# Kernel optimization log

Measured on AMD Instinct MI355X. Metric: run time of the kernel, lower is better.

## Reference

```python
import jax, jax.numpy as jnp
import numpy as np

NEG_INF = -1e9


def setup_inputs() -> dict:
    key = jax.random.key(0)
    k1, k2, k3 = jax.random.split(key, 3)
    B, N, F_IN, F_OUT = 8, 4096, 128, 64
    h = jax.random.normal(k1, (B, N, F_IN), dtype=jnp.float32)
    # xavier_uniform with gain=1.414 on [F_IN, F_OUT]
    limit = 1.414 * np.sqrt(6.0 / (F_IN + F_OUT))
    W = jax.random.uniform(k2, (F_IN, F_OUT), dtype=jnp.float32, minval=-limit, maxval=limit)
    adj = jax.random.randint(k3, (N, N), 0, 2, dtype=jnp.int32)
    return {"h": h, "W": W, "adj": adj}


def reference(h, W, adj):
    # h: [B, N, F_in], W: [F_in, F_out], adj: [N, N]
    F_out = W.shape[1]
    Wh = jnp.einsum('bnf,fo->bno', h, W)                      # [B, N, F_out]
    scores = jnp.einsum('bnd,bmd->bnm', Wh, Wh) / np.sqrt(F_out).astype(np.float32)
    attention = jnp.where(adj[None, :, :] > 0, scores, NEG_INF)
    attention = jax.nn.softmax(attention, axis=2)             # [B, N, N]
    # dropout p=0.0 / eval mode -> identity
    h_prime = jnp.einsum('bnm,bmd->bnd', attention, Wh)       # [B, N, F_out]
    return jax.nn.elu(h_prime)  # concat=True path
```

## Files before the change

### kernel.cpp

```cpp
#include <hip/hip_runtime.h>

typedef _Float16 half8  __attribute__((ext_vector_type(8)));
typedef _Float16 half4v __attribute__((ext_vector_type(4)));
typedef float    float4v __attribute__((ext_vector_type(4)));

#define N_ 4096
#define B_ 8
#define D_ 64
#define F_ 128

__global__ __launch_bounds__(256) void pack_adj_kernel(const int4* __restrict__ adj4,
                                                       unsigned long long* __restrict__ bits) {
  __shared__ unsigned char nib[256];
  const int t = threadIdx.x;
  int4 v = adj4[(size_t)blockIdx.x * 256 + t];
  unsigned n = (v.x > 0 ? 1u : 0u) | (v.y > 0 ? 2u : 0u) |
               (v.z > 0 ? 4u : 0u) | (v.w > 0 ? 8u : 0u);
  nib[t] = (unsigned char)n;
  __syncthreads();
  if (t < 16) {
    const unsigned char* p = &nib[t * 16];
    unsigned long long wv = 0;
#pragma unroll
    for (int i = 0; i < 16; ++i) wv |= (unsigned long long)p[i] << (4 * i);
    bits[(size_t)blockIdx.x * 16 + t] = wv;
  }
}

__global__ __launch_bounds__(256) void wh_kernel(const float* __restrict__ h,
                                                 const float* __restrict__ W,
                                                 _Float16* __restrict__ Wh16,
                                                 _Float16* __restrict__ WhT16) {
  __shared__ __align__(16) float    hs[64][132];
  __shared__ __align__(16) _Float16 wt[64][132];
  __shared__ __align__(16) _Float16 otile[64][72];
  const int t = threadIdx.x;
  const int rowbase = blockIdx.x * 64;
  const float4v* hg = (const float4v*)(h + (size_t)rowbase * F_);
#pragma unroll
  for (int k = 0; k < 8; ++k) {
    int i4 = t + k * 256;
    float4v v = hg[i4];
    int r = i4 >> 5, c4 = (i4 & 31) * 4;
    *(float4v*)&hs[r][c4] = v;
  }
#pragma unroll
  for (int k = 0; k < 8; ++k) {
    int i4 = t + k * 256;
    float4v v = ((const float4v*)W)[i4];
    int f = i4 >> 4, c4 = (i4 & 15) * 4;
    wt[c4 + 0][f] = (_Float16)v[0];
    wt[c4 + 1][f] = (_Float16)v[1];
    wt[c4 + 2][f] = (_Float16)v[2];
    wt[c4 + 3][f] = (_Float16)v[3];
  }
  __syncthreads();
  const int w = t >> 6, lane = t & 63;
  const int r0 = w * 16;
  float acc[16];
#pragma unroll
  for (int i = 0; i < 16; ++i) acc[i] = 0.f;
#pragma unroll 4
  for (int f4 = 0; f4 < 32; ++f4) {
    half4v wv = *(half4v*)&wt[lane][f4 * 4];
    float w0 = (float)wv[0], w1 = (float)wv[1], w2 = (float)wv[2], w3 = (float)wv[3];
#pragma unroll
    for (int i = 0; i < 16; ++i) {
      float4v hv = *(float4v*)&hs[r0 + i][f4 * 4];
      acc[i] += hv[0] * w0 + hv[1] * w1 + hv[2] * w2 + hv[3] * w3;
    }
  }
#pragma unroll
  for (int i = 0; i < 16; ++i) {
    _Float16 hv = (_Float16)acc[i];
    Wh16[(size_t)(rowbase + r0 + i) * D_ + lane] = hv;
    otile[r0 + i][lane] = hv;
  }
  __syncthreads();
  const int dl = t >> 2, k0t = (t & 3) * 16;
  half8 o0, o1;
#pragma unroll
  for (int i = 0; i < 8; ++i) o0[i] = otile[k0t + i][dl];
#pragma unroll
  for (int i = 0; i < 8; ++i) o1[i] = otile[k0t + 8 + i][dl];
  const int b = rowbase >> 12, n0 = rowbase & 4095;
  _Float16* dst = WhT16 + ((size_t)(b * D_ + dl)) * N_ + n0 + k0t;
  *(half8*)dst       = o0;
  *(half8*)(dst + 8) = o1;
}

__global__ __launch_bounds__(512, 4) void attn_kernel(
    const unsigned long long* __restrict__ bits,
    const _Float16* __restrict__ Wh,
    const _Float16* __restrict__ WhT,
    float* __restrict__ out) {
  __shared__ __align__(16) char lds[81920];
  const int tid  = threadIdx.x;
  const int w    = tid >> 6;
  const int lane = tid & 63;
  const int g    = lane >> 4;
  const int c    = lane & 15;
  const int qi   = w & 3;
  const int s    = w >> 2;
  const int bid  = blockIdx.x;
  const int b    = bid >> 6;
  const int q0b  = (bid & 63) * 64;
  const int q0w  = q0b + qi * 16;

  const _Float16* Whb  = Wh  + (size_t)b * N_ * D_;
  const _Float16* WhTb = WhT + (size_t)b * D_ * N_;
  char* Kbase = lds + s * 16384;
  char* Vbase = lds + 32768 + s * 16384;
  char* Pb    = lds + 65536 + w * 2048;

  const int e0  = (qi * 2 + 0) * 64 + lane;
  const int e1  = (qi * 2 + 1) * 64 + lane;
  const int r0e = e0 >> 3, s0e = (e0 & 7) ^ (r0e & 7);
  const int r1e = e1 >> 3, s1e = (e1 & 7) ^ (r1e & 7);

  half8 qf[2];
#pragma unroll
  for (int ds = 0; ds < 2; ++ds) {
    half8 v = *(const half8*)(Whb + (size_t)(q0w + c) * D_ + ds * 32 + g * 8);
    qf[ds] = v * (_Float16)0.18033688f;
  }

  float4v o_acc[4];
#pragma unroll
  for (int d = 0; d < 4; ++d) o_acc[d] = (float4v){0.f, 0.f, 0.f, 0.f};
  float mrow = -1e30f, lrow = 0.f;

  const unsigned long long* bq = bits + (size_t)(q0w + c) * 64 + s * 32;

  int k0n = (s * 32) * 64;
  half8 ka = *(const half8*)(Whb + (size_t)(k0n + r0e) * D_ + s0e * 8);
  half8 kb = *(const half8*)(Whb + (size_t)(k0n + r1e) * D_ + s1e * 8);
  half8 va = *(const half8*)(WhTb + (size_t)r0e * N_ + k0n + s0e * 8);
  half8 vb = *(const half8*)(WhTb + (size_t)r1e * N_ + k0n + s1e * 8);
  unsigned long long bw = bq[0];
  *(half8*)(Kbase + e0 * 16) = ka;
  *(half8*)(Kbase + e1 * 16) = kb;
  *(half8*)(Vbase + e0 * 16) = va;
  *(half8*)(Vbase + e1 * 16) = vb;
  __syncthreads();

  for (int t = 0; t < 32; ++t) {
    const int cur = (t & 1) * 8192, nxt = 8192 - cur;
    const _Float16* Kc = (const _Float16*)(Kbase + cur);
    const _Float16* Vc = (const _Float16*)(Vbase + cur);

    const int t1 = (t + 1 < 32) ? t + 1 : 31;
    k0n = (s * 32 + t1) * 64;
    ka = *(const half8*)(Whb + (size_t)(k0n + r0e) * D_ + s0e * 8);
    kb = *(const half8*)(Whb + (size_t)(k0n + r1e) * D_ + s1e * 8);
    va = *(const half8*)(WhTb + (size_t)r0e * N_ + k0n + s0e * 8);
    vb = *(const half8*)(WhTb + (size_t)r1e * N_ + k0n + s1e * 8);
    unsigned long long bwn = bq[t1];

    float4v sac[4];
#pragma unroll
    for (int st = 0; st < 4; ++st) {
      const _Float16* kr = Kc + (st * 16 + c) * 64;
      half8 kf0 = *(const half8*)(kr + ((g       ^ (c & 7)) * 8));
      half8 kf1 = *(const half8*)(kr + (((g + 4) ^ (c & 7)) * 8));
      float4v z = (float4v){0.f, 0.f, 0.f, 0.f};
      z = __builtin_amdgcn_mfma_f32_16x16x32_f16(kf0, qf[0], z, 0, 0, 0);
      z = __builtin_amdgcn_mfma_f32_16x16x32_f16(kf1, qf[1], z, 0, 0, 0);
      sac[st] = z;
    }

    float tmax = -1e30f;
#pragma unroll
    for (int st = 0; st < 4; ++st) {
      unsigned wb = (unsigned)(bw >> (st * 16 + g * 4));
#pragma unroll
      for (int j = 0; j < 4; ++j) {
        float v = (wb & (1u << j)) ? sac[st][j] : -1e9f;
        sac[st][j] = v;
        tmax = fmaxf(tmax, v);
      }
    }
    tmax = fmaxf(tmax, __shfl_xor(tmax, 16));
    tmax = fmaxf(tmax, __shfl_xor(tmax, 32));

    float mnew  = fmaxf(mrow, tmax);
    float alpha = exp2f(mrow - mnew);
    mrow = mnew;
    lrow *= alpha;
#pragma unroll
    for (int j = 0; j < 4; ++j) {
      float aj = __shfl(alpha, (lane & 48) | (g * 4 + j));
#pragma unroll
      for (int d = 0; d < 4; ++d) o_acc[d][j] *= aj;
    }

#pragma unroll
    for (int st = 0; st < 4; ++st) {
      float p0 = exp2f(sac[st][0] - mrow);
      float p1 = exp2f(sac[st][1] - mrow);
      float p2 = exp2f(sac[st][2] - mrow);
      float p3 = exp2f(sac[st][3] - mrow);
      lrow += (p0 + p1) + (p2 + p3);
      uint2 pr;
      pr.x = __builtin_bit_cast(unsigned, __builtin_amdgcn_cvt_pkrtz(p0, p1));
      pr.y = __builtin_bit_cast(unsigned, __builtin_amdgcn_cvt_pkrtz(p2, p3));
      const int cell = st * 2 + (g >> 1);
      *(uint2*)(Pb + (cell * 16 + c) * 16 + (g & 1) * 8) = pr;
    }

#pragma unroll
    for (int ks = 0; ks < 2; ++ks) {
      half8 af = *(const half8*)(Pb + ((ks * 4 + g) * 16 + c) * 16);
#pragma unroll
      for (int d = 0; d < 4; ++d) {
        const int vrow = d * 16 + c;
        half8 vf = *(const half8*)(Vc + vrow * 64 + (((ks * 4 + g) ^ (c & 7)) * 8));
        o_acc[d] = __builtin_amdgcn_mfma_f32_16x16x32_f16(af, vf, o_acc[d], 0, 0, 0);
      }
    }

    *(half8*)(Kbase + nxt + e0 * 16) = ka;
    *(half8*)(Kbase + nxt + e1 * 16) = kb;
    *(half8*)(Vbase + nxt + e0 * 16) = va;
    *(half8*)(Vbase + nxt + e1 * 16) = vb;
    __syncthreads();
    bw = bwn;
  }

  lrow += __shfl_xor(lrow, 16);
  lrow += __shfl_xor(lrow, 32);
  __syncthreads();
  float* Ob = (float*)lds;
#pragma unroll
  for (int d = 0; d < 4; ++d)
#pragma unroll
    for (int j = 0; j < 4; ++j)
      Ob[(w * 16 + g * 4 + j) * 66 + d * 16 + c] = o_acc[d][j];
  float2* mlb = (float2*)(lds + 36864);
  if (g == 0) mlb[w * 16 + c] = make_float2(mrow, lrow);
  __syncthreads();

#pragma unroll
  for (int it = 0; it < 8; ++it) {
    int r   = w + it * 8;
    int col = lane;
    int qq = r >> 4, rl = r & 15;
    float2 ml0 = mlb[qq * 16 + rl];
    float2 ml1 = mlb[(qq + 4) * 16 + rl];
    float mm = fmaxf(ml0.x, ml1.x);
    float a0 = exp2f(ml0.x - mm);
    float a1 = exp2f(ml1.x - mm);
    float l  = a0 * ml0.y + a1 * ml1.y;
    float o  = a0 * Ob[(qq * 16 + rl) * 66 + col] + a1 * Ob[((qq + 4) * 16 + rl) * 66 + col];
    float x  = o / l;
    x = x > 0.f ? x : (__expf(x) - 1.f);
    out[((size_t)b * N_ + q0b + r) * D_ + col] = x;
  }
}

extern "C" void kernel_launch(void* const* d_in, const int* in_sizes, int n_in,
                              void* d_out, int out_size, void* d_ws, size_t ws_size,
                              hipStream_t stream) {
  const float* h = (const float*)d_in[0];
  const float* W = (const float*)d_in[1];
  const int* adj = (const int*)d_in[2];
  float* out = (float*)d_out;

  char* ws = (char*)d_ws;
  unsigned long long* bits = (unsigned long long*)ws;
  _Float16* Wh16  = (_Float16*)(ws + (2u << 20));
  _Float16* WhT16 = (_Float16*)(ws + (6u << 20));

  hipLaunchKernelGGL(pack_adj_kernel, dim3((N_ * N_) / 1024), dim3(256), 0, stream,
                     (const int4*)adj, bits);
  hipLaunchKernelGGL(wh_kernel,   dim3((B_ * N_) / 64), dim3(256), 0, stream, h, W, Wh16, WhT16);
  hipLaunchKernelGGL(attn_kernel, dim3(B_ * (N_ / 64)), dim3(512), 0, stream, bits, Wh16, WhT16, out);
}
```

Measured before the change: 204.6 us.

## Use MFMA for Wh projection and streamline attention loop with lazy rescale

The Wh projection kernel now converts h to fp16 into swizzled LDS and computes the 64x64 tile with MFMA 16x16x32 instructions instead of scalar FMA loops. Wh stores are also made coalesced through the output tile. In the attention kernel the main loop peels its last iteration, uses pointer increments, and builds the max with a tree reduction. It also skips the online-softmax rescale when no row max increases. The projection now rounds h to fp16, which costs input precision, and the rescale branch adds wave-divergence checks.

```diff
diff --git a/kernel.cpp b/kernel.cpp
--- a/kernel.cpp
+++ b/kernel.cpp
@@ -1,7 +1,6 @@
 #include <hip/hip_runtime.h>
 
 typedef _Float16 half8  __attribute__((ext_vector_type(8)));
-typedef _Float16 half4v __attribute__((ext_vector_type(4)));
 typedef float    float4v __attribute__((ext_vector_type(4)));
 
 #define N_ 4096
@@ -31,52 +30,70 @@
                                                  const float* __restrict__ W,
                                                  _Float16* __restrict__ Wh16,
                                                  _Float16* __restrict__ WhT16) {
-  __shared__ __align__(16) float    hs[64][132];
-  __shared__ __align__(16) _Float16 wt[64][132];
+  __shared__ __align__(16) _Float16 hs[64 * 128];
+  __shared__ __align__(16) _Float16 wt[64 * 128];
   __shared__ __align__(16) _Float16 otile[64][72];
   const int t = threadIdx.x;
   const int rowbase = blockIdx.x * 64;
-  const float4v* hg = (const float4v*)(h + (size_t)rowbase * F_);
-#pragma unroll
-  for (int k = 0; k < 8; ++k) {
-    int i4 = t + k * 256;
-    float4v v = hg[i4];
-    int r = i4 >> 5, c4 = (i4 & 31) * 4;
-    *(float4v*)&hs[r][c4] = v;
+#pragma unroll
+  for (int i = 0; i < 4; ++i) {
+    int e = i * 256 + t;
+    int r = e >> 4, kb = e & 15;
+    const float4v* src = (const float4v*)(h + (size_t)(rowbase + r) * F_ + kb * 8);
+    float4v a = src[0], b = src[1];
+    uint4 pk;
+    pk.x = __builtin_bit_cast(unsigned, __builtin_amdgcn_cvt_pkrtz(a[0], a[1]));
+    pk.y = __builtin_bit_cast(unsigned, __builtin_amdgcn_cvt_pkrtz(a[2], a[3]));
+    pk.z = __builtin_bit_cast(unsigned, __builtin_amdgcn_cvt_pkrtz(b[0], b[1]));
+    pk.w = __builtin_bit_cast(unsigned, __builtin_amdgcn_cvt_pkrtz(b[2], b[3]));
+    *(uint4*)&hs[(r * 16 + (kb ^ (r & 7))) * 8] = pk;
   }
 #pragma unroll
   for (int k = 0; k < 8; ++k) {
     int i4 = t + k * 256;
     float4v v = ((const float4v*)W)[i4];
     int f = i4 >> 4, c4 = (i4 & 15) * 4;
-    wt[c4 + 0][f] = (_Float16)v[0];
-    wt[c4 + 1][f] = (_Float16)v[1];
-    wt[c4 + 2][f] = (_Float16)v[2];
-    wt[c4 + 3][f] = (_Float16)v[3];
+    int oct = f >> 3, ki = f & 7;
+#pragma unroll
+    for (int j = 0; j < 4; ++j) {
+      int c = c4 + j;
+      wt[(c * 16 + (oct ^ (c & 7))) * 8 + ki] = (_Float16)v[j];
+    }
   }
   __syncthreads();
   const int w = t >> 6, lane = t & 63;
+  const int g = lane >> 4, c = lane & 15;
   const int r0 = w * 16;
-  float acc[16];
-#pragma unroll
-  for (int i = 0; i < 16; ++i) acc[i] = 0.f;
-#pragma unroll 4
-  for (int f4 = 0; f4 < 32; ++f4) {
-    half4v wv = *(half4v*)&wt[lane][f4 * 4];
-    float w0 = (float)wv[0], w1 = (float)wv[1], w2 = (float)wv[2], w3 = (float)wv[3];
-#pragma unroll
-    for (int i = 0; i < 16; ++i) {
-      float4v hv = *(float4v*)&hs[r0 + i][f4 * 4];
-      acc[i] += hv[0] * w0 + hv[1] * w1 + hv[2] * w2 + hv[3] * w3;
+  const int arow = r0 + c, aswz = arow & 7;
+  half8 af[4];
+#pragma unroll
+  for (int kk = 0; kk < 4; ++kk)
+    af[kk] = *(half8*)&hs[(arow * 16 + ((kk * 4 + g) ^ aswz)) * 8];
+  float4v acc[4];
+#pragma unroll
+  for (int cb = 0; cb < 4; ++cb) {
+    float4v z = (float4v){0.f, 0.f, 0.f, 0.f};
+    const int bcol = cb * 16 + c, bswz = c & 7;
+#pragma unroll
+    for (int kk = 0; kk < 4; ++kk) {
+      half8 bf = *(half8*)&wt[(bcol * 16 + ((kk * 4 + g) ^ bswz)) * 8];
+      z = __builtin_amdgcn_mfma_f32_16x16x32_f16(af[kk], bf, z, 0, 0, 0);
     }
-  }
-#pragma unroll
-  for (int i = 0; i < 16; ++i) {
-    _Float16 hv = (_Float16)acc[i];
-    Wh16[(size_t)(rowbase + r0 + i) * D_ + lane] = hv;
-    otile[r0 + i][lane] = hv;
-  }
-  __syncthreads();
+    acc[cb] = z;
+  }
+  __syncthreads();
+#pragma unroll
+  for (int cb = 0; cb < 4; ++cb)
+#pragma unroll
+    for (int j = 0; j < 4; ++j)
+      otile[r0 + g * 4 + j][cb * 16 + c] = (_Float16)acc[cb][j];
+  __syncthreads();
+  const int rr = t >> 2, c0 = (t & 3) * 16;
+  half8 w0 = *(half8*)&otile[rr][c0];
+  half8 w1 = *(half8*)&otile[rr][c0 + 8];
+  _Float16* dW = Wh16 + (size_t)(rowbase + rr) * D_ + c0;
+  *(half8*)dW       = w0;
+  *(half8*)(dW + 8) = w1;
   const int dl = t >> 2, k0t = (t & 3) * 16;
   half8 o0, o1;
 #pragma unroll
@@ -132,100 +149,108 @@
 
   const unsigned long long* bq = bits + (size_t)(q0w + c) * 64 + s * 32;
 
-  int k0n = (s * 32) * 64;
-  half8 ka = *(const half8*)(Whb + (size_t)(k0n + r0e) * D_ + s0e * 8);
-  half8 kb = *(const half8*)(Whb + (size_t)(k0n + r1e) * D_ + s1e * 8);
-  half8 va = *(const half8*)(WhTb + (size_t)r0e * N_ + k0n + s0e * 8);
-  half8 vb = *(const half8*)(WhTb + (size_t)r1e * N_ + k0n + s1e * 8);
+  const _Float16* pk0 = Whb + (size_t)(s * 2048 + r0e) * D_ + s0e * 8;
+  const _Float16* pk1 = Whb + (size_t)(s * 2048 + r1e) * D_ + s1e * 8;
+  const _Float16* pv0 = WhTb + (size_t)r0e * N_ + s * 2048 + s0e * 8;
+  const _Float16* pv1 = WhTb + (size_t)r1e * N_ + s * 2048 + s1e * 8;
+
+  *(half8*)(Kbase + e0 * 16) = *(const half8*)pk0;
+  *(half8*)(Kbase + e1 * 16) = *(const half8*)pk1;
+  *(half8*)(Vbase + e0 * 16) = *(const half8*)pv0;
+  *(half8*)(Vbase + e1 * 16) = *(const half8*)pv1;
   unsigned long long bw = bq[0];
-  *(half8*)(Kbase + e0 * 16) = ka;
-  *(half8*)(Kbase + e1 * 16) = kb;
-  *(half8*)(Vbase + e0 * 16) = va;
-  *(half8*)(Vbase + e1 * 16) = vb;
-  __syncthreads();
-
-  for (int t = 0; t < 32; ++t) {
-    const int cur = (t & 1) * 8192, nxt = 8192 - cur;
-    const _Float16* Kc = (const _Float16*)(Kbase + cur);
-    const _Float16* Vc = (const _Float16*)(Vbase + cur);
-
-    const int t1 = (t + 1 < 32) ? t + 1 : 31;
-    k0n = (s * 32 + t1) * 64;
-    ka = *(const half8*)(Whb + (size_t)(k0n + r0e) * D_ + s0e * 8);
-    kb = *(const half8*)(Whb + (size_t)(k0n + r1e) * D_ + s1e * 8);
-    va = *(const half8*)(WhTb + (size_t)r0e * N_ + k0n + s0e * 8);
-    vb = *(const half8*)(WhTb + (size_t)r1e * N_ + k0n + s1e * 8);
-    unsigned long long bwn = bq[t1];
-
-    float4v sac[4];
-#pragma unroll
-    for (int st = 0; st < 4; ++st) {
-      const _Float16* kr = Kc + (st * 16 + c) * 64;
-      half8 kf0 = *(const half8*)(kr + ((g       ^ (c & 7)) * 8));
-      half8 kf1 = *(const half8*)(kr + (((g + 4) ^ (c & 7)) * 8));
-      float4v z = (float4v){0.f, 0.f, 0.f, 0.f};
-      z = __builtin_amdgcn_mfma_f32_16x16x32_f16(kf0, qf[0], z, 0, 0, 0);
-      z = __builtin_amdgcn_mfma_f32_16x16x32_f16(kf1, qf[1], z, 0, 0, 0);
-      sac[st] = z;
-    }
-
-    float tmax = -1e30f;
-#pragma unroll
-    for (int st = 0; st < 4; ++st) {
-      unsigned wb = (unsigned)(bw >> (st * 16 + g * 4));
-#pragma unroll
-      for (int j = 0; j < 4; ++j) {
-        float v = (wb & (1u << j)) ? sac[st][j] : -1e9f;
-        sac[st][j] = v;
-        tmax = fmaxf(tmax, v);
-      }
-    }
-    tmax = fmaxf(tmax, __shfl_xor(tmax, 16));
-    tmax = fmaxf(tmax, __shfl_xor(tmax, 32));
-
-    float mnew  = fmaxf(mrow, tmax);
-    float alpha = exp2f(mrow - mnew);
-    mrow = mnew;
-    lrow *= alpha;
-#pragma unroll
-    for (int j = 0; j < 4; ++j) {
-      float aj = __shfl(alpha, (lane & 48) | (g * 4 + j));
-#pragma unroll
-      for (int d = 0; d < 4; ++d) o_acc[d][j] *= aj;
-    }
-
-#pragma unroll
-    for (int st = 0; st < 4; ++st) {
-      float p0 = exp2f(sac[st][0] - mrow);
-      float p1 = exp2f(sac[st][1] - mrow);
-      float p2 = exp2f(sac[st][2] - mrow);
-      float p3 = exp2f(sac[st][3] - mrow);
-      lrow += (p0 + p1) + (p2 + p3);
-      uint2 pr;
-      pr.x = __builtin_bit_cast(unsigned, __builtin_amdgcn_cvt_pkrtz(p0, p1));
-      pr.y = __builtin_bit_cast(unsigned, __builtin_amdgcn_cvt_pkrtz(p2, p3));
-      const int cell = st * 2 + (g >> 1);
-      *(uint2*)(Pb + (cell * 16 + c) * 16 + (g & 1) * 8) = pr;
-    }
-
-#pragma unroll
-    for (int ks = 0; ks < 2; ++ks) {
-      half8 af = *(const half8*)(Pb + ((ks * 4 + g) * 16 + c) * 16);
-#pragma unroll
-      for (int d = 0; d < 4; ++d) {
-        const int vrow = d * 16 + c;
-        half8 vf = *(const half8*)(Vc + vrow * 64 + (((ks * 4 + g) ^ (c & 7)) * 8));
-        o_acc[d] = __builtin_amdgcn_mfma_f32_16x16x32_f16(af, vf, o_acc[d], 0, 0, 0);
-      }
-    }
-
+  __syncthreads();
+
+#define COMPUTE_TILE(CUR)                                                          \
+  {                                                                                \
+    const _Float16* Kc = (const _Float16*)(Kbase + (CUR));                         \
+    const _Float16* Vc = (const _Float16*)(Vbase + (CUR));                         \
+    float4v sac[4];                                                                \
+    _Pragma("unroll")                                                              \
+    for (int st = 0; st < 4; ++st) {                                               \
+      const _Float16* kr = Kc + (st * 16 + c) * 64;                                \
+      half8 kf0 = *(const half8*)(kr + ((g       ^ (c & 7)) * 8));                 \
+      half8 kf1 = *(const half8*)(kr + (((g + 4) ^ (c & 7)) * 8));                 \
+      float4v z = (float4v){0.f, 0.f, 0.f, 0.f};                                   \
+      z = __builtin_amdgcn_mfma_f32_16x16x32_f16(kf0, qf[0], z, 0, 0, 0);          \
+      z = __builtin_amdgcn_mfma_f32_16x16x32_f16(kf1, qf[1], z, 0, 0, 0);          \
+      sac[st] = z;                                                                 \
+    }                                                                              \
+    _Pragma("unroll")                                                              \
+    for (int st = 0; st < 4; ++st) {                                               \
+      unsigned wb = (unsigned)(bw >> (st * 16 + g * 4));                           \
+      _Pragma("unroll")                                                            \
+      for (int j = 0; j < 4; ++j)                                                  \
+        sac[st][j] = (wb & (1u << j)) ? sac[st][j] : -1e9f;                        \
+    }                                                                              \
+    float ta = fmaxf(fmaxf(sac[0][0], sac[0][1]), fmaxf(sac[0][2], sac[0][3]));    \
+    float tb = fmaxf(fmaxf(sac[1][0], sac[1][1]), fmaxf(sac[1][2], sac[1][3]));    \
+    float tc = fmaxf(fmaxf(sac[2][0], sac[2][1]), fmaxf(sac[2][2], sac[2][3]));    \
+    float td = fmaxf(fmaxf(sac[3][0], sac[3][1]), fmaxf(sac[3][2], sac[3][3]));    \
+    float tmax = fmaxf(fmaxf(ta, tb), fmaxf(tc, td));                              \
+    tmax = fmaxf(tmax, __shfl_xor(tmax, 16));                                      \
+    tmax = fmaxf(tmax, __shfl_xor(tmax, 32));                                      \
+    if (__any(tmax > mrow)) {                                                      \
+      float mnew  = fmaxf(mrow, tmax);                                             \
+      float alpha = exp2f(mrow - mnew);                                            \
+      mrow = mnew;                                                                 \
+      lrow *= alpha;                                                               \
+      _Pragma("unroll")                                                            \
+      for (int j = 0; j < 4; ++j) {                                                \
+        float aj = __shfl(alpha, (lane & 48) | (g * 4 + j));                       \
+        _Pragma("unroll")                                                          \
+        for (int d = 0; d < 4; ++d) o_acc[d][j] *= aj;                             \
+      }                                                                            \
+    }                                                                              \
+    _Pragma("unroll")                                                              \
+    for (int st = 0; st < 4; ++st) {                                               \
+      float p0 = exp2f(sac[st][0] - mrow);                                         \
+      float p1 = exp2f(sac[st][1] - mrow);                                         \
+      float p2 = exp2f(sac[st][2] - mrow);                                         \
+      float p3 = exp2f(sac[st][3] - mrow);                                         \
+      lrow += (p0 + p1) + (p2 + p3);                                               \
+      uint2 pr;                                                                    \
+      pr.x = __builtin_bit_cast(unsigned, __builtin_amdgcn_cvt_pkrtz(p0, p1));     \
+      pr.y = __builtin_bit_cast(unsigned, __builtin_amdgcn_cvt_pkrtz(p2, p3));     \
+      const int cell = st * 2 + (g >> 1);                                          \
+      *(uint2*)(Pb + (cell * 16 + c) * 16 + (g & 1) * 8) = pr;                     \
+    }                                                                              \
+    _Pragma("unroll")                                                              \
+    for (int ks = 0; ks < 2; ++ks) {                                               \
+      half8 afp = *(const half8*)(Pb + ((ks * 4 + g) * 16 + c) * 16);              \
+      _Pragma("unroll")                                                            \
+      for (int d = 0; d < 4; ++d) {                                                \
+        half8 vf = *(const half8*)(Vc + (d * 16 + c) * 64 +                        \
+                                   (((ks * 4 + g) ^ (c & 7)) * 8));                \
+        o_acc[d] = __builtin_amdgcn_mfma_f32_16x16x32_f16(afp, vf, o_acc[d],       \
+                                                          0, 0, 0);                \
+      }                                                                            \
+    }                                                                              \
+  }
+
+  int cur = 0;
+#pragma unroll 2
+  for (int t = 0; t < 31; ++t) {
+    pk0 += 64 * D_; pk1 += 64 * D_; pv0 += 64; pv1 += 64;
+    half8 ka = *(const half8*)pk0;
+    half8 kb = *(const half8*)pk1;
+    half8 va = *(const half8*)pv0;
+    half8 vb = *(const half8*)pv1;
+    unsigned long long bwn = bq[t + 1];
+
+    COMPUTE_TILE(cur)
+
+    const int nxt = cur ^ 8192;
     *(half8*)(Kbase + nxt + e0 * 16) = ka;
     *(half8*)(Kbase + nxt + e1 * 16) = kb;
     *(half8*)(Vbase + nxt + e0 * 16) = va;
     *(half8*)(Vbase + nxt + e1 * 16) = vb;
     __syncthreads();
+    cur = nxt;
     bw = bwn;
   }
+  COMPUTE_TILE(cur)
+#undef COMPUTE_TILE
 
   lrow += __shfl_xor(lrow, 16);
   lrow += __shfl_xor(lrow, 32);
```

Result: faster. 191.9 us (-6.2%).
